# Performance work log

Hardware: AMD Instinct MI355X
Metric: run time of the kernel (lower is better)

The kernel has to match this reference:

```python
import jax, jax.numpy as jnp
import numpy as np

B, N, C, NH = 4, 2304, 256, 8
HD = C // NH            # head dim = 32
HS = WS = 48            # H = W = sqrt(N)
RADIUS = 3.0
MLP_HID = 4 * C
SCALE = HD ** (-0.5)
NEG = -1e9              # stands in for -inf (identical softmax up to fp eps)
EPS = 1e-6


def spatial_mask():
    # get_spatial_mask: cdist of (y, x) grid coords, -inf where dist > radius
    yy, xx = jnp.meshgrid(jnp.arange(HS), jnp.arange(WS), indexing='ij')
    coords = jnp.stack([yy, xx], -1).reshape(-1, 2).astype(jnp.float32)  # [N, 2]
    d2 = jnp.sum((coords[:, None, :] - coords[None, :, :]) ** 2, -1)     # [N, N]
    return jnp.where(d2 > RADIUS * RADIUS, NEG, 0.0)


def layernorm(x, g, b):
    mu = jnp.mean(x, -1, keepdims=True)
    var = jnp.mean((x - mu) ** 2, -1, keepdims=True)
    return (x - mu) * jax.lax.rsqrt(var + EPS) * g + b


def setup_inputs() -> dict:
    key = jax.random.key(0)
    ks = jax.random.split(key, 16)
    s = 0.02
    return {
        'x':    jax.random.normal(ks[0], (B, N, C), jnp.float32),
        'x_kv': jax.random.normal(ks[1], (B, N, C), jnp.float32),
        'Wq': jax.random.normal(ks[2], (C, C), jnp.float32) * s,
        'bq': jnp.zeros((C,), jnp.float32),
        'Wk': jax.random.normal(ks[3], (C, C), jnp.float32) * s,
        'bk': jnp.zeros((C,), jnp.float32),
        'Wv': jax.random.normal(ks[4], (C, C), jnp.float32) * s,
        'bv': jnp.zeros((C,), jnp.float32),
        'Wp': jax.random.normal(ks[5], (C, C), jnp.float32) * s,
        'bp': jnp.zeros((C,), jnp.float32),
        'g1': jnp.ones((C,), jnp.float32),
        'b1': jnp.zeros((C,), jnp.float32),
        'g2': jnp.ones((C,), jnp.float32),
        'b2': jnp.zeros((C,), jnp.float32),
        'W1': jax.random.normal(ks[6], (C, MLP_HID), jnp.float32) * s,
        'bm1': jnp.zeros((MLP_HID,), jnp.float32),
        'W2': jax.random.normal(ks[7], (MLP_HID, C), jnp.float32) * s,
        'bm2': jnp.zeros((C,), jnp.float32),
    }


def reference(x, x_kv, Wq, bq, Wk, bk, Wv, bv, Wp, bp,
              g1, b1, g2, b2, W1, bm1, W2, bm2):
    mask = spatial_mask()                                  # [N, N]
    h = layernorm(x, g1, b1)
    hkv = layernorm(x_kv, g1, b1)
    q = (h @ Wq + bq).reshape(B, N, NH, HD)
    k = (hkv @ Wk + bk).reshape(B, N, NH, HD)
    v = (hkv @ Wv + bv).reshape(B, N, NH, HD)
    scores = jnp.einsum('bqhd,bkhd->bhqk', q, k) * SCALE + mask
    attn = jax.nn.softmax(scores, axis=-1)
    out = jnp.einsum('bhqk,bkhd->bqhd', attn, v).reshape(B, N, C)
    x = x + out @ Wp + bp
    m = layernorm(x, g2, b2)
    x = x + jax.nn.gelu(m @ W1 + bm1, approximate=False) @ W2 + bm2
    return x
```

## Files before the change

### kernel.cpp

```cpp
#include <hip/hip_runtime.h>
#include <hip/hip_fp16.h>
#include <math.h>

#define BB 4
#define NN 2304
#define CC 256
#define HS 48
#define HID 1024
#define BNROWS (BB * NN)
#define ATTN_SCALE 0.17677669529663687f

typedef _Float16 f16;
typedef __attribute__((ext_vector_type(2))) _Float16 h2;
typedef __attribute__((ext_vector_type(8))) _Float16 h8;
typedef __attribute__((ext_vector_type(4))) float f4;

#define GLLS16(g, l)                                                        \
    __builtin_amdgcn_global_load_lds(                                       \
        (const __attribute__((address_space(1))) unsigned int*)(g),         \
        (__attribute__((address_space(3))) unsigned int*)(l), 16, 0, 0)
#define WAIT_VM0()   asm volatile("s_waitcnt vmcnt(0)" ::: "memory")
#define WAIT_VM4()   asm volatile("s_waitcnt vmcnt(4)" ::: "memory")
#define WAIT_VM5()   asm volatile("s_waitcnt vmcnt(5)" ::: "memory")
#define WAIT_VM6()   asm volatile("s_waitcnt vmcnt(6)" ::: "memory")
#define WAIT_LGKM0() asm volatile("s_waitcnt lgkmcnt(0)" ::: "memory")

static __device__ __forceinline__ float wave_sum64(float v) {
    v += __shfl_xor(v, 32, 64);
    v += __shfl_xor(v, 16, 64);
    v += __shfl_xor(v, 8, 64);
    v += __shfl_xor(v, 4, 64);
    v += __shfl_xor(v, 2, 64);
    v += __shfl_xor(v, 1, 64);
    return v;
}

static __device__ __forceinline__ int xcd_swizzle_lin() {
    const int gx = (int)gridDim.x;
    const int lin = (int)blockIdx.y * gx + (int)blockIdx.x;
    const int nwg = gx * (int)gridDim.y;
    return (nwg & 7) ? lin : ((lin & 7) * (nwg >> 3) + (lin >> 3));
}

__global__ __launch_bounds__(256) void prep_ln1_kernel(
    const float* __restrict__ x, const float* __restrict__ xkv,
    const float* __restrict__ Wq, const float* __restrict__ Wk,
    const float* __restrict__ Wv, const float* __restrict__ Wp,
    const float* __restrict__ W1, const float* __restrict__ W2,
    const float* __restrict__ bq, const float* __restrict__ bk,
    const float* __restrict__ bv,
    const float* __restrict__ g, const float* __restrict__ be,
    f16* __restrict__ WqkvT, f16* __restrict__ WpT,
    f16* __restrict__ W1T, f16* __restrict__ W2T, float* __restrict__ bqkv,
    f16* __restrict__ hq, f16* __restrict__ hkv)
{
    __shared__ float tt[32][33];
    int bx = blockIdx.x;
    const int tid = threadIdx.x;
    if (bx < 768) {
        const float* src; f16* dst; int K, N;
        if (bx < 64)        { src = Wq; dst = WqkvT;           K = 256;  N = 256; }
        else if (bx < 128)  { src = Wk; dst = WqkvT + 65536;   K = 256;  N = 256;  bx -= 64; }
        else if (bx < 192)  { src = Wv; dst = WqkvT + 131072;  K = 256;  N = 256;  bx -= 128; }
        else if (bx < 256)  { src = Wp; dst = WpT;             K = 256;  N = 256;  bx -= 192; }
        else if (bx < 512)  { src = W1; dst = W1T;             K = 256;  N = 1024; bx -= 256; }
        else                { src = W2; dst = W2T;             K = 1024; N = 256;  bx -= 512; }
        const int tN = N >> 5;
        const int kt = bx / tN, nt = bx - kt * tN;
        const int rr = tid >> 5, cc = tid & 31;
#pragma unroll
        for (int j = 0; j < 4; ++j)
            tt[rr + 8 * j][cc] = src[(size_t)(kt * 32 + rr + 8 * j) * N + nt * 32 + cc];
        __syncthreads();
#pragma unroll
        for (int j = 0; j < 4; ++j)
            dst[(size_t)(nt * 32 + rr + 8 * j) * K + kt * 32 + cc] = (f16)tt[cc][rr + 8 * j];
        return;
    }
    if (bx == 768) {
        if (tid < 256) {
            bqkv[tid]       = bq[tid];
            bqkv[tid + 256] = bk[tid];
            bqkv[tid + 512] = bv[tid];
        }
        return;
    }
    const int r = (bx - 769) * 4 + (tid >> 6);
    const int lane = tid & 63;
    const float* src; f16* dst;
    if (r < BNROWS) { src = x + (size_t)r * CC;              dst = hq + (size_t)r * CC; }
    else { src = xkv + (size_t)(r - BNROWS) * CC; dst = hkv + (size_t)(r - BNROWS) * CC; }
    const float4 v = ((const float4*)src)[lane];
    const float mu = wave_sum64(v.x + v.y + v.z + v.w) * (1.0f / CC);
    const float d0 = v.x - mu, d1 = v.y - mu, d2 = v.z - mu, d3 = v.w - mu;
    const float var = wave_sum64(d0 * d0 + d1 * d1 + d2 * d2 + d3 * d3) * (1.0f / CC);
    const float rs = rsqrtf(var + 1e-6f);
    const float4 g4 = ((const float4*)g)[lane];
    const float4 b4 = ((const float4*)be)[lane];
    h2 o01 = (h2){(f16)(d0 * rs * g4.x + b4.x), (f16)(d1 * rs * g4.y + b4.y)};
    h2 o23 = (h2){(f16)(d2 * rs * g4.z + b4.z), (f16)(d3 * rs * g4.w + b4.w)};
    ((h2*)dst)[lane * 2] = o01;
    ((h2*)dst)[lane * 2 + 1] = o23;
}

template <bool GELU, int RESID, bool OUTF32, bool QKV>
__global__ __launch_bounds__(256, 4) void gemm_wave(
    const f16* __restrict__ Aq, const f16* __restrict__ Akv,
    const f16* __restrict__ Bt, const float* __restrict__ bias,
    const void* __restrict__ resid, void* __restrict__ out1,
    void* __restrict__ outkv, int N, int K)
{
    __shared__ f16 lds[4 * 6144];
    const int tid = threadIdx.x;
    const int wid = tid >> 6, lane = tid & 63;
    const int ln15 = lane & 15, quad = lane >> 4;
    const int jr = lane >> 2, js = lane & 3;
    f16* slot = lds + wid * 6144;
    const int sl = xcd_swizzle_lin();
    const int gx = (int)gridDim.x;
    const int bx = sl % gx, by = sl / gx;
    const int n0 = bx * 64;
    const int m0 = (by * 4 + wid) * 32;
    const f16* Ap = QKV ? (n0 < 256 ? Aq : Akv) : Aq;

    size_t ga[2], gb[4];
#pragma unroll
    for (int i = 0; i < 2; ++i) {
        const int r = i * 16 + jr;
        const int q = (js - (r >> 1)) & 3;
        ga[i] = (size_t)(m0 + r) * K + q * 8;
    }
#pragma unroll
    for (int i = 0; i < 4; ++i) {
        const int r = i * 16 + jr;
        const int q = (js - (r >> 1)) & 3;
        gb[i] = (size_t)(n0 + r) * K + q * 8;
    }
    int aoff[2], boff[4];
#pragma unroll
    for (int mt = 0; mt < 2; ++mt) {
        const int r = mt * 16 + ln15;
        aoff[mt] = (r * 4 + ((quad + (r >> 1)) & 3)) * 16;
    }
#pragma unroll
    for (int nt = 0; nt < 4; ++nt) {
        const int r = nt * 16 + ln15;
        boff[nt] = (r * 4 + ((quad + (r >> 1)) & 3)) * 16;
    }

    f4 acc[2][4];
#pragma unroll
    for (int i = 0; i < 2; ++i)
#pragma unroll
        for (int j = 0; j < 4; ++j) acc[i][j] = (f4){0.f, 0.f, 0.f, 0.f};

    {
        f16* Al = slot;
        f16* Bl = slot + 1024;
#pragma unroll
        for (int i = 0; i < 2; ++i) GLLS16(Ap + ga[i], Al + i * 512);
#pragma unroll
        for (int i = 0; i < 4; ++i) GLLS16(Bt + gb[i], Bl + i * 512);
    }

    int cur = 0;
    for (int k0 = 0; k0 < K; k0 += 32) {
        const bool more = (k0 + 32 < K);
        f16* Ac = slot + cur * 3072;
        f16* Bc = Ac + 1024;
        if (more) {
            f16* An = slot + (cur ^ 1) * 3072;
            f16* Bn = An + 1024;
            WAIT_LGKM0();
#pragma unroll
            for (int i = 0; i < 2; ++i) GLLS16(Ap + ga[i] + k0 + 32, An + i * 512);
#pragma unroll
            for (int i = 0; i < 4; ++i) GLLS16(Bt + gb[i] + k0 + 32, Bn + i * 512);
            WAIT_VM6();
        } else {
            WAIT_VM0();
        }
        h8 aF[2], bF[4];
#pragma unroll
        for (int nt = 0; nt < 4; ++nt)
            bF[nt] = *(const h8*)((const char*)Bc + boff[nt]);
#pragma unroll
        for (int mt = 0; mt < 2; ++mt)
            aF[mt] = *(const h8*)((const char*)Ac + aoff[mt]);
#pragma unroll
        for (int mt = 0; mt < 2; ++mt)
#pragma unroll
            for (int nt = 0; nt < 4; ++nt)
                acc[mt][nt] = __builtin_amdgcn_mfma_f32_16x16x32_f16(
                    aF[mt], bF[nt], acc[mt][nt], 0, 0, 0);
        cur ^= 1;
    }

    f16* qdst = nullptr; int qstr = 0, qn0 = 0;
    if (QKV) {
        if (n0 < 256) { qdst = (f16*)out1;  qstr = 256; qn0 = n0; }
        else          { qdst = (f16*)outkv; qstr = 512; qn0 = n0 - 256; }
    }
#pragma unroll
    for (int nt = 0; nt < 4; ++nt) {
        const int gn = n0 + nt * 16 + ln15;
        const float bs = bias[gn];
#pragma unroll
        for (int mt = 0; mt < 2; ++mt) {
#pragma unroll
            for (int r = 0; r < 4; ++r) {
                const int gm = m0 + mt * 16 + quad * 4 + r;
                float v = acc[mt][nt][r] + bs;
                if (GELU) v = 0.5f * v * (1.0f + erff(v * 0.70710678118654752f));
                if (RESID == 1) v += ((const float*)resid)[(size_t)gm * N + gn];
                if (RESID == 2) v += (float)((const f16*)resid)[(size_t)gm * N + gn];
                if (QKV) {
                    qdst[(size_t)gm * qstr + qn0 + nt * 16 + ln15] = (f16)v;
                } else if (OUTF32) {
                    ((float*)out1)[(size_t)gm * N + gn] = v;
                } else {
                    ((f16*)out1)[(size_t)gm * N + gn] = (f16)v;
                }
            }
        }
    }
}

__global__ __launch_bounds__(256, 4) void gemm_op_ln2(
    const f16* __restrict__ Aa, const f16* __restrict__ Bt,
    const float* __restrict__ bias, const float* __restrict__ xres,
    const float* __restrict__ g, const float* __restrict__ be,
    f16* __restrict__ x1, f16* __restrict__ m2)
{
    __shared__ f16 lds[4 * 5120];
    __shared__ float sred[16][4][2];
    const int tid = threadIdx.x;
    const int wid = tid >> 6, lane = tid & 63;
    const int ln15 = lane & 15, quad = lane >> 4;
    const int jr = lane >> 2, js = lane & 3;
    f16* slot = lds + wid * 5120;
    const int m0 = blockIdx.x * 16;
    const int n0 = wid * 64;
    const int K = 256;

    size_t ga, gb[4];
    {
        const int q = (js - (jr >> 1)) & 3;
        ga = (size_t)(m0 + jr) * K + q * 8;
    }
#pragma unroll
    for (int i = 0; i < 4; ++i) {
        const int r = i * 16 + jr;
        const int q = (js - (r >> 1)) & 3;
        gb[i] = (size_t)(n0 + r) * K + q * 8;
    }
    const int aoff = (ln15 * 4 + ((quad + (ln15 >> 1)) & 3)) * 16;
    int boff[4];
#pragma unroll
    for (int nt = 0; nt < 4; ++nt) {
        const int r = nt * 16 + ln15;
        boff[nt] = (r * 4 + ((quad + (r >> 1)) & 3)) * 16;
    }

    f4 acc[4];
#pragma unroll
    for (int j = 0; j < 4; ++j) acc[j] = (f4){0.f, 0.f, 0.f, 0.f};

    {
        f16* Al = slot;
        f16* Bl = slot + 512;
        GLLS16(Aa + ga, Al);
#pragma unroll
        for (int i = 0; i < 4; ++i) GLLS16(Bt + gb[i], Bl + i * 512);
    }
    int cur = 0;
    for (int k0 = 0; k0 < K; k0 += 32) {
        const bool more = (k0 + 32 < K);
        f16* Ac = slot + cur * 2560;
        f16* Bc = Ac + 512;
        if (more) {
            f16* An = slot + (cur ^ 1) * 2560;
            f16* Bn = An + 512;
            WAIT_LGKM0();
            GLLS16(Aa + ga + k0 + 32, An);
#pragma unroll
            for (int i = 0; i < 4; ++i) GLLS16(Bt + gb[i] + k0 + 32, Bn + i * 512);
            WAIT_VM5();
        } else {
            WAIT_VM0();
        }
        h8 aF, bF[4];
#pragma unroll
        for (int nt = 0; nt < 4; ++nt)
            bF[nt] = *(const h8*)((const char*)Bc + boff[nt]);
        aF = *(const h8*)((const char*)Ac + aoff);
#pragma unroll
        for (int nt = 0; nt < 4; ++nt)
            acc[nt] = __builtin_amdgcn_mfma_f32_16x16x32_f16(
                aF, bF[nt], acc[nt], 0, 0, 0);
        cur ^= 1;
    }

    float bsv[4], g2v[4], b2v[4];
#pragma unroll
    for (int nt = 0; nt < 4; ++nt) {
        const int gn = n0 + nt * 16 + ln15;
        bsv[nt] = bias[gn];
        g2v[nt] = g[gn];
        b2v[nt] = be[gn];
    }
    float s1[4], s2[4];
#pragma unroll
    for (int r = 0; r < 4; ++r) { s1[r] = 0.f; s2[r] = 0.f; }
#pragma unroll
    for (int r = 0; r < 4; ++r) {
        const int gm = m0 + quad * 4 + r;
#pragma unroll
        for (int nt = 0; nt < 4; ++nt) {
            const int gn = n0 + nt * 16 + ln15;
            float v = acc[nt][r] + bsv[nt] + xres[(size_t)gm * CC + gn];
            acc[nt][r] = v;
            x1[(size_t)gm * CC + gn] = (f16)v;
            s1[r] += v;
            s2[r] += v * v;
        }
    }
#pragma unroll
    for (int off = 1; off < 16; off <<= 1) {
#pragma unroll
        for (int r = 0; r < 4; ++r) {
            s1[r] += __shfl_xor(s1[r], off, 64);
            s2[r] += __shfl_xor(s2[r], off, 64);
        }
    }
    if (ln15 == 0) {
#pragma unroll
        for (int r = 0; r < 4; ++r) {
            const int rr = quad * 4 + r;
            sred[rr][wid][0] = s1[r];
            sred[rr][wid][1] = s2[r];
        }
    }
    __syncthreads();
#pragma unroll
    for (int r = 0; r < 4; ++r) {
        const int rr = quad * 4 + r;
        const int gm = m0 + rr;
        float a = 0.f, b = 0.f;
#pragma unroll
        for (int w = 0; w < 4; ++w) {
            a += sred[rr][w][0];
            b += sred[rr][w][1];
        }
        const float mu = a * (1.0f / CC);
        const float var = fmaxf(b * (1.0f / CC) - mu * mu, 0.0f);
        const float rs = rsqrtf(var + 1e-6f);
#pragma unroll
        for (int nt = 0; nt < 4; ++nt) {
            const int gn = n0 + nt * 16 + ln15;
            const float v = acc[nt][r];
            m2[(size_t)gm * CC + gn] = (f16)((v - mu) * rs * g2v[nt] + b2v[nt]);
        }
    }
}

__global__ __launch_bounds__(256, 2) void mlp_fused(
    const f16* __restrict__ m2g, const f16* __restrict__ W1T,
    const f16* __restrict__ W2T, const float* __restrict__ bm1,
    const float* __restrict__ bm2, const f16* __restrict__ x1,
    float* __restrict__ outp)
{
    __shared__ f16 lds[4 * 6144];
    __shared__ f16 hbuf[32 * 512];
    const int tid = threadIdx.x;
    const int wid = tid >> 6, lane = tid & 63;
    const int ln15 = lane & 15, quad = lane >> 4;
    const int jr = lane >> 2, js = lane & 3;
    f16* slot = lds + wid * 6144;
    const int m0 = blockIdx.x * 32;

    size_t ga[2];
#pragma unroll
    for (int i = 0; i < 2; ++i) {
        const int r = i * 16 + jr;
        const int q = (js - (r >> 1)) & 3;
        ga[i] = (size_t)(m0 + r) * 256 + q * 8;
    }
    size_t gb1[2][4];
#pragma unroll
    for (int nt2 = 0; nt2 < 2; ++nt2)
#pragma unroll
        for (int i = 0; i < 4; ++i) {
            const int r = i * 16 + jr;
            const int q = (js - (r >> 1)) & 3;
            gb1[nt2][i] = (size_t)(wid * 128 + nt2 * 64 + r) * 256 + q * 8;
        }
    size_t gb2[4];
#pragma unroll
    for (int i = 0; i < 4; ++i) {
        const int r = i * 16 + jr;
        const int q = (js - (r >> 1)) & 3;
        gb2[i] = (size_t)(wid * 64 + r) * 1024 + q * 8;
    }
    int aoff[2], boff[4];
#pragma unroll
    for (int mt = 0; mt < 2; ++mt) {
        const int r = mt * 16 + ln15;
        aoff[mt] = (r * 4 + ((quad + (r >> 1)) & 3)) * 16;
    }
#pragma unroll
    for (int nt = 0; nt < 4; ++nt) {
        const int r = nt * 16 + ln15;
        boff[nt] = (r * 4 + ((quad + (r >> 1)) & 3)) * 16;
    }

    f4 acc2[2][4];
#pragma unroll
    for (int i = 0; i < 2; ++i)
#pragma unroll
        for (int j = 0; j < 4; ++j) acc2[i][j] = (f4){0.f, 0.f, 0.f, 0.f};

#pragma unroll 1
    for (int half = 0; half < 2; ++half) {
        const size_t bofs1 = (size_t)half * 512 * 256;
        {
            f16* Al = slot;
            f16* Bl = slot + 1024;
#pragma unroll
            for (int i = 0; i < 2; ++i) GLLS16(m2g + ga[i], Al + i * 512);
#pragma unroll
            for (int i = 0; i < 4; ++i) GLLS16(W1T + gb1[0][i] + bofs1, Bl + i * 512);
        }
        int cur = 0;
        f4 accp[2][4];
#pragma unroll 1
        for (int it = 0; it < 16; ++it) {
            const int ntile = it >> 3;
            f16* Ac = slot + cur * 3072;
            f16* Bc = Ac + 1024;
            if (it < 15) {
                const int itn = it + 1;
                const int ntn = itn >> 3, k0n = (itn & 7) * 32;
                f16* An = slot + (cur ^ 1) * 3072;
                f16* Bn = An + 1024;
                WAIT_LGKM0();
#pragma unroll
                for (int i = 0; i < 2; ++i)
                    GLLS16(m2g + ga[i] + k0n, An + i * 512);
#pragma unroll
                for (int i = 0; i < 4; ++i)
                    GLLS16(W1T + gb1[ntn][i] + bofs1 + k0n, Bn + i * 512);
                WAIT_VM6();
            } else {
                WAIT_VM0();
            }
            if ((it & 7) == 0) {
#pragma unroll
                for (int i = 0; i < 2; ++i)
#pragma unroll
                    for (int j = 0; j < 4; ++j) accp[i][j] = (f4){0.f, 0.f, 0.f, 0.f};
            }
            h8 aF[2], bF[4];
#pragma unroll
            for (int nt = 0; nt < 4; ++nt)
                bF[nt] = *(const h8*)((const char*)Bc + boff[nt]);
#pragma unroll
            for (int mt = 0; mt < 2; ++mt)
                aF[mt] = *(const h8*)((const char*)Ac + aoff[mt]);
#pragma unroll
            for (int mt = 0; mt < 2; ++mt)
#pragma unroll
                for (int nt = 0; nt < 4; ++nt)
                    accp[mt][nt] = __builtin_amdgcn_mfma_f32_16x16x32_f16(
                        aF[mt], bF[nt], accp[mt][nt], 0, 0, 0);
            if ((it & 7) == 7) {
#pragma unroll
                for (int mt = 0; mt < 2; ++mt)
#pragma unroll
                    for (int nt = 0; nt < 4; ++nt)
#pragma unroll
                        for (int r = 0; r < 4; ++r) {
                            const int row = mt * 16 + quad * 4 + r;
                            const int col = wid * 128 + ntile * 64 + nt * 16 + ln15;
                            float v = accp[mt][nt][r] + bm1[half * 512 + col];
                            v = 0.5f * v * (1.0f + erff(v * 0.70710678118654752f));
                            const int sw = (col >> 3) ^ (row & 7);
                            hbuf[row * 512 + sw * 8 + (col & 7)] = (f16)v;
                        }
            }
            cur ^= 1;
        }
        __syncthreads();
        {
            f16* Bl = slot;
#pragma unroll
            for (int i = 0; i < 4; ++i)
                GLLS16(W2T + gb2[i] + half * 512, Bl + i * 512);
        }
        cur = 0;
#pragma unroll 1
        for (int it = 0; it < 16; ++it) {
            f16* Bc = slot + cur * 2048;
            if (it < 15) {
                f16* Bn = slot + (cur ^ 1) * 2048;
                WAIT_LGKM0();
#pragma unroll
                for (int i = 0; i < 4; ++i)
                    GLLS16(W2T + gb2[i] + half * 512 + (it + 1) * 32, Bn + i * 512);
                WAIT_VM4();
            } else {
                WAIT_VM0();
            }
            h8 bF[4];
#pragma unroll
            for (int nt = 0; nt < 4; ++nt)
                bF[nt] = *(const h8*)((const char*)Bc + boff[nt]);
            h8 aF[2];
#pragma unroll
            for (int mt = 0; mt < 2; ++mt) {
                const int row = mt * 16 + ln15;
                const int sw = (it * 4 + quad) ^ (row & 7);
                aF[mt] = *(const h8*)&hbuf[row * 512 + sw * 8];
            }
#pragma unroll
            for (int mt = 0; mt < 2; ++mt)
#pragma unroll
                for (int nt = 0; nt < 4; ++nt)
                    acc2[mt][nt] = __builtin_amdgcn_mfma_f32_16x16x32_f16(
                        aF[mt], bF[nt], acc2[mt][nt], 0, 0, 0);
            cur ^= 1;
        }
        if (half == 0) __syncthreads();
    }
#pragma unroll
    for (int nt = 0; nt < 4; ++nt) {
        const int gn = wid * 64 + nt * 16 + ln15;
        const float bs = bm2[gn];
#pragma unroll
        for (int mt = 0; mt < 2; ++mt) {
#pragma unroll
            for (int r = 0; r < 4; ++r) {
                const int gm = m0 + mt * 16 + quad * 4 + r;
                const float v = acc2[mt][nt][r] + bs
                              + (float)x1[(size_t)gm * CC + gn];
                outp[(size_t)gm * CC + gn] = v;
            }
        }
    }
}

__device__ __constant__ int ATT_DY[29] = {
    -3, -2, -2, -2, -2, -2, -1, -1, -1, -1, -1, 0, 0, 0, 0,
    0, 0, 0, 1, 1, 1, 1, 1, 2, 2, 2, 2, 2, 3};
__device__ __constant__ int ATT_DX[29] = {
    0, -2, -1, 0, 1, 2, -2, -1, 0, 1, 2, -3, -2, -1, 0,
    1, 2, 3, -2, -1, 0, 1, 2, -2, -1, 0, 1, 2, 0};

__global__ __launch_bounds__(128) void attn_tile_kernel(
    const f16* __restrict__ qf, const f16* __restrict__ kvf,
    f16* __restrict__ ao)
{
    __shared__ f16 ks[196][66];
    __shared__ f16 vs[196][66];
    const int tile = blockIdx.x, hp = blockIdx.y, b = blockIdx.z;
    const int ty0 = (tile / 6) * 8, tx0 = (tile - (tile / 6) * 6) * 8;
    const int tid = threadIdx.x;

    const int q = tid & 63, hh = tid >> 6;
    const int qy = q >> 3, qx = q & 7;
    const size_t qrow = (size_t)b * NN + (ty0 + qy) * HS + tx0 + qx;
    const f16* qp = qf + qrow * CC + hp * 64 + hh * 32;
    uint4 qa[4];
#pragma unroll
    for (int i = 0; i < 4; ++i) qa[i] = ((const uint4*)qp)[i];

#pragma unroll
    for (int bt = 0; bt < 5; ++bt) {
        uint4 v[5];
        int rr[5], sg[5];
#pragma unroll
        for (int j = 0; j < 5; ++j) {
            const int it = bt * 5 + j;
            const int idx = tid + it * 128;
            const int r = idx >> 4, seg = idx & 15;
            rr[j] = r; sg[j] = seg;
            const int ry = r / 14;
            const int gy = ty0 - 3 + ry, gx = tx0 - 3 + (r - ry * 14);
            uint4 val = {0u, 0u, 0u, 0u};
            const bool act = (it < 24) || (tid < 64);
            if (act && (unsigned)gy < HS && (unsigned)gx < HS) {
                const size_t rowb = ((size_t)b * NN + gy * HS + gx) * 512;
                const int ch = (seg < 8) ? (hp * 64 + seg * 8)
                                         : (256 + hp * 64 + (seg - 8) * 8);
                val = *(const uint4*)&kvf[rowb + ch];
            }
            v[j] = val;
        }
#pragma unroll
        for (int j = 0; j < 5; ++j) {
            const int it = bt * 5 + j;
            if (it == 24 && tid >= 64) continue;
            f16* dstp = (sg[j] < 8) ? &ks[rr[j]][(sg[j] & 7) * 8]
                                    : &vs[rr[j]][(sg[j] & 7) * 8];
            ((unsigned int*)dstp)[0] = v[j].x;
            ((unsigned int*)dstp)[1] = v[j].y;
            ((unsigned int*)dstp)[2] = v[j].z;
            ((unsigned int*)dstp)[3] = v[j].w;
        }
    }
    __syncthreads();

    const h2* q2 = (const h2*)qa;

    float s[29];
#pragma unroll
    for (int n = 0; n < 29; ++n) {
        const int dy = ATT_DY[n], dx = ATT_DX[n];
        const int r = (qy + 3 + dy) * 14 + qx + 3 + dx;
        const bool valid = (unsigned)(ty0 + qy + dy) < HS &&
                           (unsigned)(tx0 + qx + dx) < HS;
        float a = 0.0f;
        const h2* kp = (const h2*)&ks[r][hh * 32];
#pragma unroll
        for (int i = 0; i < 16; ++i)
            a = __builtin_amdgcn_fdot2(q2[i], kp[i], a, false);
        s[n] = valid ? a * ATTN_SCALE : -1e30f;
    }
    float m = s[0];
#pragma unroll
    for (int n = 1; n < 29; ++n) m = fmaxf(m, s[n]);
    float l = 0.0f;
#pragma unroll
    for (int n = 0; n < 29; ++n) { s[n] = __expf(s[n] - m); l += s[n]; }
    h2 a2[16];
#pragma unroll
    for (int i = 0; i < 16; ++i) a2[i] = (h2){(f16)0.f, (f16)0.f};
#pragma unroll
    for (int n = 0; n < 29; ++n) {
        const int dy = ATT_DY[n], dx = ATT_DX[n];
        const int r = (qy + 3 + dy) * 14 + qx + 3 + dx;
        const f16 pn = (f16)s[n];
        const h2 ph = (h2){pn, pn};
        const h2* vp = (const h2*)&vs[r][hh * 32];
#pragma unroll
        for (int i = 0; i < 16; ++i) a2[i] += ph * vp[i];
    }
    const float inv = 1.0f / l;
    uint4 ov[4];
    f16* oh = (f16*)ov;
#pragma unroll
    for (int i = 0; i < 16; ++i) {
        oh[2 * i]     = (f16)((float)a2[i][0] * inv);
        oh[2 * i + 1] = (f16)((float)a2[i][1] * inv);
    }
    uint4* dst = (uint4*)(ao + qrow * CC + hp * 64 + hh * 32);
#pragma unroll
    for (int i = 0; i < 4; ++i) dst[i] = ov[i];
}

extern "C" void kernel_launch(void* const* d_in, const int* in_sizes, int n_in,
                              void* d_out, int out_size, void* d_ws, size_t ws_size,
                              hipStream_t stream) {
    const float* x    = (const float*)d_in[0];
    const float* x_kv = (const float*)d_in[1];
    const float* Wq   = (const float*)d_in[2];
    const float* bq   = (const float*)d_in[3];
    const float* Wk   = (const float*)d_in[4];
    const float* bk   = (const float*)d_in[5];
    const float* Wv   = (const float*)d_in[6];
    const float* bv   = (const float*)d_in[7];
    const float* Wp   = (const float*)d_in[8];
    const float* bp   = (const float*)d_in[9];
    const float* g1   = (const float*)d_in[10];
    const float* b1   = (const float*)d_in[11];
    const float* g2   = (const float*)d_in[12];
    const float* b2   = (const float*)d_in[13];
    const float* W1   = (const float*)d_in[14];
    const float* bm1  = (const float*)d_in[15];
    const float* W2   = (const float*)d_in[16];
    const float* bm2  = (const float*)d_in[17];
    float* outp = (float*)d_out;

    f16* wsh = (f16*)d_ws;
    f16* WqkvT = wsh;
    f16* WpT   = wsh + 196608;
    f16* W1T   = wsh + 262144;
    f16* W2T   = wsh + 524288;
    float* bqkv = (float*)(wsh + 786432);
    f16* hq    = wsh + 787968;
    f16* hkv   = wsh + 3147264;
    f16* qf    = wsh + 5506560;
    f16* kvf   = wsh + 7865856;
    f16* ao    = hq;
    f16* x1    = hkv;
    f16* m2    = qf;

    prep_ln1_kernel<<<5377, 256, 0, stream>>>(
        x, x_kv, Wq, Wk, Wv, Wp, W1, W2, bq, bk, bv, g1, b1,
        WqkvT, WpT, W1T, W2T, bqkv, hq, hkv);
    gemm_wave<false, 0, false, true><<<dim3(12, 72), 256, 0, stream>>>(
        hq, hkv, WqkvT, bqkv, nullptr, qf, kvf, 768, 256);
    attn_tile_kernel<<<dim3(36, 4, BB), 128, 0, stream>>>(qf, kvf, ao);
    gemm_op_ln2<<<576, 256, 0, stream>>>(ao, WpT, bp, x, g2, b2, x1, m2);
    mlp_fused<<<288, 256, 0, stream>>>(m2, W1T, W2T, bm1, bm2, x1, outp);
    (void)in_sizes; (void)n_in; (void)out_size; (void)ws_size;
}
```

Measured before the change: 185.7 us.

## Shrink fused MLP row tile to 16 and chunk hidden dim in quarters

The fused MLP kernel now processes 16 rows per block instead of 32 and walks the 1024-wide hidden dimension in four 256-column chunks instead of two 512-column halves. This doubles the grid to 576 blocks, shrinks LDS per block, and raises the launch-bounds occupancy hint from 2 to 3 blocks per CU. The aim is to fill more of the GPU and hide latency better. The cost is that every block re-streams the full W1/W2 weights for half as many rows, doubling weight traffic through L2, and it adds more per-chunk barriers.

```diff
diff --git a/kernel.cpp b/kernel.cpp
--- a/kernel.cpp
+++ b/kernel.cpp
@@ -364,37 +364,33 @@
     }
 }
 
-__global__ __launch_bounds__(256, 2) void mlp_fused(
+__global__ __launch_bounds__(256, 3) void mlp_fused(
     const f16* __restrict__ m2g, const f16* __restrict__ W1T,
     const f16* __restrict__ W2T, const float* __restrict__ bm1,
     const float* __restrict__ bm2, const f16* __restrict__ x1,
     float* __restrict__ outp)
 {
-    __shared__ f16 lds[4 * 6144];
-    __shared__ f16 hbuf[32 * 512];
+    __shared__ f16 lds[4 * 5120];
+    __shared__ f16 hbuf[16 * 256];
     const int tid = threadIdx.x;
     const int wid = tid >> 6, lane = tid & 63;
     const int ln15 = lane & 15, quad = lane >> 4;
     const int jr = lane >> 2, js = lane & 3;
-    f16* slot = lds + wid * 6144;
-    const int m0 = blockIdx.x * 32;
-
-    size_t ga[2];
-#pragma unroll
-    for (int i = 0; i < 2; ++i) {
+    f16* slot = lds + wid * 5120;
+    const int m0 = blockIdx.x * 16;
+
+    size_t ga;
+    {
+        const int q = (js - (jr >> 1)) & 3;
+        ga = (size_t)(m0 + jr) * 256 + q * 8;
+    }
+    size_t gb1[4];
+#pragma unroll
+    for (int i = 0; i < 4; ++i) {
         const int r = i * 16 + jr;
         const int q = (js - (r >> 1)) & 3;
-        ga[i] = (size_t)(m0 + r) * 256 + q * 8;
-    }
-    size_t gb1[2][4];
-#pragma unroll
-    for (int nt2 = 0; nt2 < 2; ++nt2)
-#pragma unroll
-        for (int i = 0; i < 4; ++i) {
-            const int r = i * 16 + jr;
-            const int q = (js - (r >> 1)) & 3;
-            gb1[nt2][i] = (size_t)(wid * 128 + nt2 * 64 + r) * 256 + q * 8;
-        }
+        gb1[i] = (size_t)(wid * 64 + r) * 256 + q * 8;
+    }
     size_t gb2[4];
 #pragma unroll
     for (int i = 0; i < 4; ++i) {
@@ -402,111 +398,88 @@
         const int q = (js - (r >> 1)) & 3;
         gb2[i] = (size_t)(wid * 64 + r) * 1024 + q * 8;
     }
-    int aoff[2], boff[4];
-#pragma unroll
-    for (int mt = 0; mt < 2; ++mt) {
-        const int r = mt * 16 + ln15;
-        aoff[mt] = (r * 4 + ((quad + (r >> 1)) & 3)) * 16;
-    }
+    const int aoff = (ln15 * 4 + ((quad + (ln15 >> 1)) & 3)) * 16;
+    int boff[4];
 #pragma unroll
     for (int nt = 0; nt < 4; ++nt) {
         const int r = nt * 16 + ln15;
         boff[nt] = (r * 4 + ((quad + (r >> 1)) & 3)) * 16;
     }
 
-    f4 acc2[2][4];
-#pragma unroll
-    for (int i = 0; i < 2; ++i)
-#pragma unroll
-        for (int j = 0; j < 4; ++j) acc2[i][j] = (f4){0.f, 0.f, 0.f, 0.f};
+    f4 acc2[4];
+#pragma unroll
+    for (int j = 0; j < 4; ++j) acc2[j] = (f4){0.f, 0.f, 0.f, 0.f};
 
 #pragma unroll 1
-    for (int half = 0; half < 2; ++half) {
-        const size_t bofs1 = (size_t)half * 512 * 256;
+    for (int qt = 0; qt < 4; ++qt) {
+        const size_t w1ofs = (size_t)qt * 65536;
         {
             f16* Al = slot;
-            f16* Bl = slot + 1024;
-#pragma unroll
-            for (int i = 0; i < 2; ++i) GLLS16(m2g + ga[i], Al + i * 512);
-#pragma unroll
-            for (int i = 0; i < 4; ++i) GLLS16(W1T + gb1[0][i] + bofs1, Bl + i * 512);
+            f16* Bl = slot + 512;
+            GLLS16(m2g + ga, Al);
+#pragma unroll
+            for (int i = 0; i < 4; ++i)
+                GLLS16(W1T + gb1[i] + w1ofs, Bl + i * 512);
         }
         int cur = 0;
-        f4 accp[2][4];
+        f4 accp[4];
+#pragma unroll
+        for (int j = 0; j < 4; ++j) accp[j] = (f4){0.f, 0.f, 0.f, 0.f};
 #pragma unroll 1
-        for (int it = 0; it < 16; ++it) {
-            const int ntile = it >> 3;
-            f16* Ac = slot + cur * 3072;
-            f16* Bc = Ac + 1024;
-            if (it < 15) {
-                const int itn = it + 1;
-                const int ntn = itn >> 3, k0n = (itn & 7) * 32;
-                f16* An = slot + (cur ^ 1) * 3072;
-                f16* Bn = An + 1024;
+        for (int it = 0; it < 8; ++it) {
+            f16* Ac = slot + cur * 2560;
+            f16* Bc = Ac + 512;
+            if (it < 7) {
+                f16* An = slot + (cur ^ 1) * 2560;
+                f16* Bn = An + 512;
                 WAIT_LGKM0();
-#pragma unroll
-                for (int i = 0; i < 2; ++i)
-                    GLLS16(m2g + ga[i] + k0n, An + i * 512);
+                GLLS16(m2g + ga + (it + 1) * 32, An);
 #pragma unroll
                 for (int i = 0; i < 4; ++i)
-                    GLLS16(W1T + gb1[ntn][i] + bofs1 + k0n, Bn + i * 512);
-                WAIT_VM6();
+                    GLLS16(W1T + gb1[i] + w1ofs + (it + 1) * 32, Bn + i * 512);
+                WAIT_VM5();
             } else {
                 WAIT_VM0();
             }
-            if ((it & 7) == 0) {
-#pragma unroll
-                for (int i = 0; i < 2; ++i)
-#pragma unroll
-                    for (int j = 0; j < 4; ++j) accp[i][j] = (f4){0.f, 0.f, 0.f, 0.f};
-            }
-            h8 aF[2], bF[4];
+            h8 aF, bF[4];
 #pragma unroll
             for (int nt = 0; nt < 4; ++nt)
                 bF[nt] = *(const h8*)((const char*)Bc + boff[nt]);
-#pragma unroll
-            for (int mt = 0; mt < 2; ++mt)
-                aF[mt] = *(const h8*)((const char*)Ac + aoff[mt]);
-#pragma unroll
-            for (int mt = 0; mt < 2; ++mt)
-#pragma unroll
-                for (int nt = 0; nt < 4; ++nt)
-                    accp[mt][nt] = __builtin_amdgcn_mfma_f32_16x16x32_f16(
-                        aF[mt], bF[nt], accp[mt][nt], 0, 0, 0);
-            if ((it & 7) == 7) {
-#pragma unroll
-                for (int mt = 0; mt < 2; ++mt)
-#pragma unroll
-                    for (int nt = 0; nt < 4; ++nt)
-#pragma unroll
-                        for (int r = 0; r < 4; ++r) {
-                            const int row = mt * 16 + quad * 4 + r;
-                            const int col = wid * 128 + ntile * 64 + nt * 16 + ln15;
-                            float v = accp[mt][nt][r] + bm1[half * 512 + col];
-                            v = 0.5f * v * (1.0f + erff(v * 0.70710678118654752f));
-                            const int sw = (col >> 3) ^ (row & 7);
-                            hbuf[row * 512 + sw * 8 + (col & 7)] = (f16)v;
-                        }
+            aF = *(const h8*)((const char*)Ac + aoff);
+#pragma unroll
+            for (int nt = 0; nt < 4; ++nt)
+                accp[nt] = __builtin_amdgcn_mfma_f32_16x16x32_f16(
+                    aF, bF[nt], accp[nt], 0, 0, 0);
+            cur ^= 1;
+        }
+#pragma unroll
+        for (int nt = 0; nt < 4; ++nt)
+#pragma unroll
+            for (int r = 0; r < 4; ++r) {
+                const int row = quad * 4 + r;
+                const int col = wid * 64 + nt * 16 + ln15;
+                float v = accp[nt][r] + bm1[qt * 256 + col];
+                v = 0.5f * v * (1.0f + erff(v * 0.70710678118654752f));
+                const int sw = (col >> 3) ^ (row & 7);
+                hbuf[row * 256 + sw * 8 + (col & 7)] = (f16)v;
             }
-            cur ^= 1;
-        }
         __syncthreads();
         {
             f16* Bl = slot;
 #pragma unroll
             for (int i = 0; i < 4; ++i)
-                GLLS16(W2T + gb2[i] + half * 512, Bl + i * 512);
+                GLLS16(W2T + gb2[i] + qt * 256, Bl + i * 512);
         }
         cur = 0;
 #pragma unroll 1
-        for (int it = 0; it < 16; ++it) {
+        for (int it = 0; it < 8; ++it) {
             f16* Bc = slot + cur * 2048;
-            if (it < 15) {
+            if (it < 7) {
                 f16* Bn = slot + (cur ^ 1) * 2048;
                 WAIT_LGKM0();
 #pragma unroll
                 for (int i = 0; i < 4; ++i)
-                    GLLS16(W2T + gb2[i] + half * 512 + (it + 1) * 32, Bn + i * 512);
+                    GLLS16(W2T + gb2[i] + qt * 256 + (it + 1) * 32, Bn + i * 512);
                 WAIT_VM4();
             } else {
                 WAIT_VM0();
@@ -515,36 +488,28 @@
 #pragma unroll
             for (int nt = 0; nt < 4; ++nt)
                 bF[nt] = *(const h8*)((const char*)Bc + boff[nt]);
-            h8 aF[2];
-#pragma unroll
-            for (int mt = 0; mt < 2; ++mt) {
-                const int row = mt * 16 + ln15;
-                const int sw = (it * 4 + quad) ^ (row & 7);
-                aF[mt] = *(const h8*)&hbuf[row * 512 + sw * 8];
+            h8 aF;
+            {
+                const int g = (it * 4 + quad) ^ (ln15 & 7);
+                aF = *(const h8*)&hbuf[ln15 * 256 + g * 8];
             }
 #pragma unroll
-            for (int mt = 0; mt < 2; ++mt)
-#pragma unroll
-                for (int nt = 0; nt < 4; ++nt)
-                    acc2[mt][nt] = __builtin_amdgcn_mfma_f32_16x16x32_f16(
-                        aF[mt], bF[nt], acc2[mt][nt], 0, 0, 0);
+            for (int nt = 0; nt < 4; ++nt)
+                acc2[nt] = __builtin_amdgcn_mfma_f32_16x16x32_f16(
+                    aF, bF[nt], acc2[nt], 0, 0, 0);
             cur ^= 1;
         }
-        if (half == 0) __syncthreads();
+        if (qt < 3) __syncthreads();
     }
 #pragma unroll
     for (int nt = 0; nt < 4; ++nt) {
         const int gn = wid * 64 + nt * 16 + ln15;
         const float bs = bm2[gn];
 #pragma unroll
-        for (int mt = 0; mt < 2; ++mt) {
-#pragma unroll
-            for (int r = 0; r < 4; ++r) {
-                const int gm = m0 + mt * 16 + quad * 4 + r;
-                const float v = acc2[mt][nt][r] + bs
-                              + (float)x1[(size_t)gm * CC + gn];
-                outp[(size_t)gm * CC + gn] = v;
-            }
+        for (int r = 0; r < 4; ++r) {
+            const int gm = m0 + quad * 4 + r;
+            const float v = acc2[nt][r] + bs + (float)x1[(size_t)gm * CC + gn];
+            outp[(size_t)gm * CC + gn] = v;
         }
     }
 }
@@ -702,6 +667,6 @@
         hq, hkv, WqkvT, bqkv, nullptr, qf, kvf, 768, 256);
     attn_tile_kernel<<<dim3(36, 4, BB), 128, 0, stream>>>(qf, kvf, ao);
     gemm_op_ln2<<<576, 256, 0, stream>>>(ao, WpT, bp, x, g2, b2, x1, m2);
-    mlp_fused<<<288, 256, 0, stream>>>(m2, W1T, W2T, bm1, bm2, x1, outp);
+    mlp_fused<<<576, 256, 0, stream>>>(m2, W1T, W2T, bm1, bm2, x1, outp);
     (void)in_sizes; (void)n_in; (void)out_size; (void)ws_size;
 }
```

Result: no change. 184.9 us (-0.4%).
